# Performance work log

Hardware: AMD Instinct MI355X
Metric: run time of the kernel (lower is better)

## Reference

```python
import jax, jax.numpy as jnp
import numpy as np

TEMPERATURE = 8.0  # init_kwargs temperature
NEG_INF = -1e16


def setup_inputs() -> dict:
    key = jax.random.key(0)
    ks = jax.random.split(key, 8)
    B, S, D = 4, 1024, 64
    q = jax.random.normal(ks[0], (B, S, D), dtype=jnp.float32)
    k = jax.random.normal(ks[1], (B, S, D), dtype=jnp.float32)
    v = jax.random.normal(ks[2], (B, S, D), dtype=jnp.float32)
    # MLP params (Linear(2D,50) -> ReLU -> Linear(50,25) -> ReLU -> Linear(25,1))
    W1 = jax.random.normal(ks[3], (2 * D, 50), dtype=jnp.float32) * (1.0 / np.sqrt(2 * D))
    b1 = jnp.zeros((50,), dtype=jnp.float32)
    W2 = jax.random.normal(ks[4], (50, 25), dtype=jnp.float32) * (1.0 / np.sqrt(50))
    b2 = jnp.zeros((25,), dtype=jnp.float32)
    W3 = jax.random.normal(ks[5], (25, 1), dtype=jnp.float32) * (1.0 / np.sqrt(25))
    b3 = jnp.zeros((1,), dtype=jnp.float32)
    # causal mask: True where attention is disallowed (j > i)
    mask = jnp.triu(jnp.ones((S, S), dtype=bool), k=1)
    mask = jnp.broadcast_to(mask, (B, S, S))
    return {"q": q, "k": k, "v": v, "W1": W1, "b1": b1, "W2": W2,
            "b2": b2, "W3": W3, "b3": b3, "mask": mask}


def reference(q, k, v, W1, b1, W2, b2, W3, b3, mask):
    D = q.shape[-1]
    # cat([q_i, k_j]) @ W1 == q_i @ W1[:D] + k_j @ W1[D:]; avoids the
    # explicit [B,S,S,2D] concat the torch code materializes.
    Wq, Wk = W1[:D], W1[D:]
    hq = jnp.einsum('bsd,df->bsf', q, Wq)           # [B,S,50]
    hk = jnp.einsum('btd,df->btf', k, Wk)           # [B,S,50]
    h1 = jax.nn.relu(hq[:, :, None, :] + hk[:, None, :, :] + b1)  # [B,S,S,50]
    h2 = jax.nn.relu(jnp.einsum('bstf,fg->bstg', h1, W2) + b2)    # [B,S,S,25]
    scores = (jnp.einsum('bstg,go->bsto', h2, W3) + b3)[..., 0]    # [B,S,S]
    scores = scores / TEMPERATURE
    scores = jnp.where(mask, NEG_INF, scores)
    attn = jax.nn.softmax(scores, axis=2)           # softmax over key dim
    out = jnp.einsum('bst,btd->bsd', attn, v)       # [B,S,D]
    return (out, attn)
```

## Files before the change

kernel.cpp:

```cpp
#include <hip/hip_runtime.h>
#include <hip/hip_fp16.h>
#include <math.h>

#define BB 4
#define SQL 1024
#define DD 64
#define NFP 64
#define TEMP_INV 0.125f

typedef __attribute__((ext_vector_type(8))) _Float16 f16x8;
typedef __attribute__((ext_vector_type(4))) float f32x4;

__global__ __launch_bounds__(256) void proj_kernel(
    const float* __restrict__ q, const float* __restrict__ k,
    const float* __restrict__ W1, const float* __restrict__ b1,
    _Float16* __restrict__ hq, _Float16* __restrict__ hk)
{
  const int lane = threadIdx.x & 63;
  const int wave = threadIdx.x >> 6;
  const int unit = blockIdx.x * 4 + wave;
  const int isK  = unit >> 12;
  const int row  = unit & 4095;
  __shared__ float r[4][DD];
  const float* src = isK ? k : q;
  r[wave][lane] = src[row * DD + lane];
  __syncthreads();
  float acc = 0.f;
  if (lane < 50) {
    acc = isK ? 0.f : b1[lane];
    const float* w = W1 + isK * DD * 50 + lane;
#pragma unroll
    for (int d = 0; d < DD; ++d) acc = fmaf(r[wave][d], w[d * 50], acc);
  }
  _Float16* dst = isK ? hk : hq;
  dst[row * NFP + lane] = (_Float16)acc;
}

__global__ __launch_bounds__(512, 4) void attn_kernel(
    const _Float16* __restrict__ hq, const _Float16* __restrict__ hk,
    const float* __restrict__ v,
    const float* __restrict__ W2, const float* __restrict__ b2,
    const float* __restrict__ W3, const float* __restrict__ b3,
    float* __restrict__ out, float* __restrict__ attn)
{
  const int bid  = blockIdx.x;
  const int b    = blockIdx.y;
  const int tid  = threadIdx.x;
  const int lane = tid & 63;
  const int wave = tid >> 6;
  const int lo   = lane & 15;
  const int grp  = lane >> 4;

  __shared__ float sc[8][SQL];
  __shared__ _Float16 shq[8][NFP];

  const int sA = 4 * bid;
  const int sB = 1020 - 4 * bid;

  if (tid < 64) {
    int r = tid >> 3, c8 = (tid & 7) * 8;
    int s = (r < 4) ? (sA + r) : (sB + r - 4);
    *(float4*)(&shq[r][c8]) =
        *(const float4*)(hq + ((size_t)(b * SQL + s)) * NFP + c8);
  }

  f16x8 w2f[2][2];
#pragma unroll
  for (int gt = 0; gt < 2; ++gt) {
    int g = lo + 16 * gt;
#pragma unroll
    for (int c = 0; c < 2; ++c) {
      f16x8 fr;
#pragma unroll
      for (int j = 0; j < 8; ++j) {
        int f = c * 32 + grp * 8 + j;
        float val = (f < 50 && g < 25) ? W2[f * 25 + g] : 0.f;
        fr[j] = (_Float16)val;
      }
      w2f[gt][c] = fr;
    }
  }
  float w3a[4], w3b[4], b2a[4], b2b[4];
#pragma unroll
  for (int rr = 0; rr < 4; ++rr) {
    int g0 = grp * 4 + rr;
    int g1 = 16 + grp * 4 + rr;
    w3a[rr] = W3[g0];
    b2a[rr] = b2[g0];
    w3b[rr] = (g1 < 25) ? W3[g1] : 0.f;
    b2b[rr] = (g1 < 25) ? b2[g1] : 0.f;
  }
  const float b3v = b3[0];

  __syncthreads();

  const int smax = sB + 3;
  const int ntiles = (smax >> 5) + 1;
  const _Float16* hkb = hk + (size_t)b * SQL * NFP;

  for (int tt = wave; tt < ntiles; tt += 8) {
    const int tbase = tt << 5;
    f16x8 hkv[2][2];
#pragma unroll
    for (int th = 0; th < 2; ++th) {
      const _Float16* p = hkb + (size_t)(tbase + th * 16 + lo) * NFP + grp * 8;
#pragma unroll
      for (int c = 0; c < 2; ++c)
        hkv[th][c] = *(const f16x8*)(p + c * 32);
    }
#pragma unroll 1
    for (int r = 0; r < 8; ++r) {
      const int s = (r < 4) ? (sA + r) : (sB + r - 4);
      if (s < tbase) continue;
      f16x8 hqv[2];
#pragma unroll
      for (int c = 0; c < 2; ++c)
        hqv[c] = *(const f16x8*)(&shq[r][c * 32 + grp * 8]);
      f32x4 acc[2][2] = {{{0.f,0.f,0.f,0.f},{0.f,0.f,0.f,0.f}},
                         {{0.f,0.f,0.f,0.f},{0.f,0.f,0.f,0.f}}};
#pragma unroll
      for (int th = 0; th < 2; ++th) {
#pragma unroll
        for (int c = 0; c < 2; ++c) {
          f16x8 h = hqv[c] + hkv[th][c];
          f16x8 bfrag = __builtin_elementwise_max(h, (f16x8)0);
          acc[th][0] = __builtin_amdgcn_mfma_f32_16x16x32_f16(w2f[0][c], bfrag, acc[th][0], 0, 0, 0);
          acc[th][1] = __builtin_amdgcn_mfma_f32_16x16x32_f16(w2f[1][c], bfrag, acc[th][1], 0, 0, 0);
        }
      }
#pragma unroll
      for (int th = 0; th < 2; ++th) {
        float part = 0.f;
#pragma unroll
        for (int rr = 0; rr < 4; ++rr) {
          part += fmaxf(acc[th][0][rr] + b2a[rr], 0.f) * w3a[rr];
          part += fmaxf(acc[th][1][rr] + b2b[rr], 0.f) * w3b[rr];
        }
        part += __shfl_xor(part, 16);
        part += __shfl_xor(part, 32);
        float score = (part + b3v) * TEMP_INV;
        if (lane < 16) sc[r][tbase + th * 16 + lane] = score;
      }
    }
  }

  __syncthreads();

  {
    const int r = wave;
    const int s = (r < 4) ? (sA + r) : (sB + r - 4);
    float vv[16];
#pragma unroll
    for (int c = 0; c < 16; ++c) {
      int t = c * 64 + lane;
      vv[c] = (t <= s) ? sc[r][t] : -INFINITY;
    }
    float m = vv[0];
#pragma unroll
    for (int c = 1; c < 16; ++c) m = fmaxf(m, vv[c]);
#pragma unroll
    for (int off = 32; off; off >>= 1) m = fmaxf(m, __shfl_xor(m, off));
    float sum = 0.f;
#pragma unroll
    for (int c = 0; c < 16; ++c) {
      float e = (c * 64 + lane <= s) ? __expf(vv[c] - m) : 0.f;
      vv[c] = e;
      sum += e;
    }
#pragma unroll
    for (int off = 32; off; off >>= 1) sum += __shfl_xor(sum, off);
    const float inv = 1.f / sum;
    float* arow = attn + ((size_t)(b * SQL + s)) * SQL;
#pragma unroll
    for (int c = 0; c < 16; ++c) {
      float a = vv[c] * inv;
      arow[c * 64 + lane] = a;
      sc[r][c * 64 + lane] = a;
    }
    const float* vb = v + (size_t)(b * SQL) * DD + lane;
    float a0 = 0.f, a1 = 0.f, a2 = 0.f, a3 = 0.f;
    int t = 0;
    for (; t + 3 <= s; t += 4) {
      a0 = fmaf(sc[r][t],     vb[(size_t)(t)     * DD], a0);
      a1 = fmaf(sc[r][t + 1], vb[(size_t)(t + 1) * DD], a1);
      a2 = fmaf(sc[r][t + 2], vb[(size_t)(t + 2) * DD], a2);
      a3 = fmaf(sc[r][t + 3], vb[(size_t)(t + 3) * DD], a3);
    }
    for (; t <= s; ++t) a0 = fmaf(sc[r][t], vb[(size_t)t * DD], a0);
    out[((size_t)(b * SQL + s)) * DD + lane] = (a0 + a1) + (a2 + a3);
  }
}

extern "C" void kernel_launch(void* const* d_in, const int* in_sizes, int n_in,
                              void* d_out, int out_size, void* d_ws, size_t ws_size,
                              hipStream_t stream) {
  const float* q  = (const float*)d_in[0];
  const float* k  = (const float*)d_in[1];
  const float* v  = (const float*)d_in[2];
  const float* W1 = (const float*)d_in[3];
  const float* b1 = (const float*)d_in[4];
  const float* W2 = (const float*)d_in[5];
  const float* b2 = (const float*)d_in[6];
  const float* W3 = (const float*)d_in[7];
  const float* b3 = (const float*)d_in[8];

  float* out  = (float*)d_out;
  float* attn = out + BB * SQL * DD;

  _Float16* hq = (_Float16*)d_ws;
  _Float16* hk = hq + BB * SQL * NFP;

  proj_kernel<<<dim3(2048), 256, 0, stream>>>(q, k, W1, b1, hq, hk);
  attn_kernel<<<dim3(128, BB), 512, 0, stream>>>(hq, hk, v, W2, b2, W3, b3, out, attn);
}
```

Measured before the change: 177.0 us.

## Split attention into score and softmax-PV kernels with global score buffer

The fused attention kernel becomes two kernels. The score kernel spreads the key tiles of each block over twice as many blocks and handles the low and high query rows of a pair together, so each loaded hk tile is reused. It writes scores to a global workspace buffer. A new per-row kernel then does softmax and the PV product with 256 threads, splitting the key range across waves. This removes the serial single-wave softmax/PV tail and the large shared score array, but adds a 16 MB round trip to global memory and one more launch.

Measured after the change: 155.9 us. 1.14x faster.

```diff
diff --git a/kernel.cpp b/kernel.cpp
--- a/kernel.cpp
+++ b/kernel.cpp
@@ -25,33 +25,35 @@
   const float* src = isK ? k : q;
   r[wave][lane] = src[row * DD + lane];
   __syncthreads();
-  float acc = 0.f;
+  float acc0 = 0.f, acc1 = 0.f;
   if (lane < 50) {
-    acc = isK ? 0.f : b1[lane];
+    acc0 = isK ? 0.f : b1[lane];
     const float* w = W1 + isK * DD * 50 + lane;
 #pragma unroll
-    for (int d = 0; d < DD; ++d) acc = fmaf(r[wave][d], w[d * 50], acc);
+    for (int d = 0; d < DD; d += 2) {
+      acc0 = fmaf(r[wave][d],     w[d * 50],       acc0);
+      acc1 = fmaf(r[wave][d + 1], w[(d + 1) * 50], acc1);
+    }
   }
   _Float16* dst = isK ? hk : hq;
-  dst[row * NFP + lane] = (_Float16)acc;
-}
-
-__global__ __launch_bounds__(512, 4) void attn_kernel(
+  dst[row * NFP + lane] = (_Float16)(acc0 + acc1);
+}
+
+__global__ __launch_bounds__(512, 4) void score_kernel(
     const _Float16* __restrict__ hq, const _Float16* __restrict__ hk,
-    const float* __restrict__ v,
     const float* __restrict__ W2, const float* __restrict__ b2,
     const float* __restrict__ W3, const float* __restrict__ b3,
-    float* __restrict__ out, float* __restrict__ attn)
+    float* __restrict__ sc_g)
 {
   const int bid  = blockIdx.x;
-  const int b    = blockIdx.y;
+  const int half = blockIdx.y;
+  const int b    = blockIdx.z;
   const int tid  = threadIdx.x;
   const int lane = tid & 63;
   const int wave = tid >> 6;
   const int lo   = lane & 15;
   const int grp  = lane >> 4;
 
-  __shared__ float sc[8][SQL];
   __shared__ _Float16 shq[8][NFP];
 
   const int sA = 4 * bid;
@@ -94,11 +96,10 @@
 
   __syncthreads();
 
-  const int smax = sB + 3;
-  const int ntiles = (smax >> 5) + 1;
+  const int ntiles = ((sB + 3) >> 5) + 1;
   const _Float16* hkb = hk + (size_t)b * SQL * NFP;
 
-  for (int tt = wave; tt < ntiles; tt += 8) {
+  for (int tt = wave + (half << 3); tt < ntiles; tt += 16) {
     const int tbase = tt << 5;
     f16x8 hkv[2][2];
 #pragma unroll
@@ -109,86 +110,145 @@
         hkv[th][c] = *(const f16x8*)(p + c * 32);
     }
 #pragma unroll 1
-    for (int r = 0; r < 8; ++r) {
-      const int s = (r < 4) ? (sA + r) : (sB + r - 4);
-      if (s < tbase) continue;
-      f16x8 hqv[2];
+    for (int pr = 0; pr < 4; ++pr) {
+      const int s_h = sB + pr;
+      if (s_h < tbase) continue;
+      const int s_l = sA + pr;
+      const bool has_l = (s_l >= tbase);
+
+      f16x8 hqh[2], hql[2];
 #pragma unroll
       for (int c = 0; c < 2; ++c)
-        hqv[c] = *(const f16x8*)(&shq[r][c * 32 + grp * 8]);
-      f32x4 acc[2][2] = {{{0.f,0.f,0.f,0.f},{0.f,0.f,0.f,0.f}},
-                         {{0.f,0.f,0.f,0.f},{0.f,0.f,0.f,0.f}}};
+        hqh[c] = *(const f16x8*)(&shq[pr + 4][c * 32 + grp * 8]);
+      if (has_l) {
+#pragma unroll
+        for (int c = 0; c < 2; ++c)
+          hql[c] = *(const f16x8*)(&shq[pr][c * 32 + grp * 8]);
+      }
+
+      f32x4 acch[2][2] = {{{0.f,0.f,0.f,0.f},{0.f,0.f,0.f,0.f}},
+                          {{0.f,0.f,0.f,0.f},{0.f,0.f,0.f,0.f}}};
+      f32x4 accl[2][2] = {{{0.f,0.f,0.f,0.f},{0.f,0.f,0.f,0.f}},
+                          {{0.f,0.f,0.f,0.f},{0.f,0.f,0.f,0.f}}};
 #pragma unroll
       for (int th = 0; th < 2; ++th) {
 #pragma unroll
         for (int c = 0; c < 2; ++c) {
-          f16x8 h = hqv[c] + hkv[th][c];
-          f16x8 bfrag = __builtin_elementwise_max(h, (f16x8)0);
-          acc[th][0] = __builtin_amdgcn_mfma_f32_16x16x32_f16(w2f[0][c], bfrag, acc[th][0], 0, 0, 0);
-          acc[th][1] = __builtin_amdgcn_mfma_f32_16x16x32_f16(w2f[1][c], bfrag, acc[th][1], 0, 0, 0);
+          f16x8 bh = __builtin_elementwise_max(hqh[c] + hkv[th][c], (f16x8)0);
+          acch[th][0] = __builtin_amdgcn_mfma_f32_16x16x32_f16(w2f[0][c], bh, acch[th][0], 0, 0, 0);
+          acch[th][1] = __builtin_amdgcn_mfma_f32_16x16x32_f16(w2f[1][c], bh, acch[th][1], 0, 0, 0);
+          if (has_l) {
+            f16x8 bl = __builtin_elementwise_max(hql[c] + hkv[th][c], (f16x8)0);
+            accl[th][0] = __builtin_amdgcn_mfma_f32_16x16x32_f16(w2f[0][c], bl, accl[th][0], 0, 0, 0);
+            accl[th][1] = __builtin_amdgcn_mfma_f32_16x16x32_f16(w2f[1][c], bl, accl[th][1], 0, 0, 0);
+          }
         }
       }
+      float sh[2], sl[2];
 #pragma unroll
       for (int th = 0; th < 2; ++th) {
         float part = 0.f;
 #pragma unroll
         for (int rr = 0; rr < 4; ++rr) {
-          part += fmaxf(acc[th][0][rr] + b2a[rr], 0.f) * w3a[rr];
-          part += fmaxf(acc[th][1][rr] + b2b[rr], 0.f) * w3b[rr];
+          part += fmaxf(acch[th][0][rr] + b2a[rr], 0.f) * w3a[rr];
+          part += fmaxf(acch[th][1][rr] + b2b[rr], 0.f) * w3b[rr];
         }
         part += __shfl_xor(part, 16);
         part += __shfl_xor(part, 32);
-        float score = (part + b3v) * TEMP_INV;
-        if (lane < 16) sc[r][tbase + th * 16 + lane] = score;
-      }
-    }
-  }
-
-  __syncthreads();
-
-  {
-    const int r = wave;
-    const int s = (r < 4) ? (sA + r) : (sB + r - 4);
-    float vv[16];
-#pragma unroll
-    for (int c = 0; c < 16; ++c) {
-      int t = c * 64 + lane;
-      vv[c] = (t <= s) ? sc[r][t] : -INFINITY;
-    }
-    float m = vv[0];
-#pragma unroll
-    for (int c = 1; c < 16; ++c) m = fmaxf(m, vv[c]);
-#pragma unroll
-    for (int off = 32; off; off >>= 1) m = fmaxf(m, __shfl_xor(m, off));
-    float sum = 0.f;
-#pragma unroll
-    for (int c = 0; c < 16; ++c) {
-      float e = (c * 64 + lane <= s) ? __expf(vv[c] - m) : 0.f;
-      vv[c] = e;
-      sum += e;
-    }
-#pragma unroll
-    for (int off = 32; off; off >>= 1) sum += __shfl_xor(sum, off);
-    const float inv = 1.f / sum;
-    float* arow = attn + ((size_t)(b * SQL + s)) * SQL;
-#pragma unroll
-    for (int c = 0; c < 16; ++c) {
-      float a = vv[c] * inv;
-      arow[c * 64 + lane] = a;
-      sc[r][c * 64 + lane] = a;
-    }
-    const float* vb = v + (size_t)(b * SQL) * DD + lane;
-    float a0 = 0.f, a1 = 0.f, a2 = 0.f, a3 = 0.f;
-    int t = 0;
-    for (; t + 3 <= s; t += 4) {
-      a0 = fmaf(sc[r][t],     vb[(size_t)(t)     * DD], a0);
-      a1 = fmaf(sc[r][t + 1], vb[(size_t)(t + 1) * DD], a1);
-      a2 = fmaf(sc[r][t + 2], vb[(size_t)(t + 2) * DD], a2);
-      a3 = fmaf(sc[r][t + 3], vb[(size_t)(t + 3) * DD], a3);
-    }
-    for (; t <= s; ++t) a0 = fmaf(sc[r][t], vb[(size_t)t * DD], a0);
-    out[((size_t)(b * SQL + s)) * DD + lane] = (a0 + a1) + (a2 + a3);
-  }
+        sh[th] = (part + b3v) * TEMP_INV;
+      }
+      if (lane < 32)
+        sc_g[((size_t)(b * SQL + s_h) << 10) + tbase + lane] = (lane & 16) ? sh[1] : sh[0];
+      if (has_l) {
+#pragma unroll
+        for (int th = 0; th < 2; ++th) {
+          float part = 0.f;
+#pragma unroll
+          for (int rr = 0; rr < 4; ++rr) {
+            part += fmaxf(accl[th][0][rr] + b2a[rr], 0.f) * w3a[rr];
+            part += fmaxf(accl[th][1][rr] + b2b[rr], 0.f) * w3b[rr];
+          }
+          part += __shfl_xor(part, 16);
+          part += __shfl_xor(part, 32);
+          sl[th] = (part + b3v) * TEMP_INV;
+        }
+        if (lane < 32)
+          sc_g[((size_t)(b * SQL + s_l) << 10) + tbase + lane] = (lane & 16) ? sl[1] : sl[0];
+      }
+    }
+  }
+}
+
+__global__ __launch_bounds__(256) void smpv_kernel(
+    const float* __restrict__ sc_g, const float* __restrict__ v,
+    float* __restrict__ out, float* __restrict__ attn)
+{
+  const int s    = blockIdx.x;
+  const int b    = blockIdx.y;
+  const int tid  = threadIdx.x;
+  const int lane = tid & 63;
+  const int wave = tid >> 6;
+
+  __shared__ float sp[SQL];
+  __shared__ float red[2][4];
+  __shared__ float outred[4][DD];
+
+  const float* srow = sc_g + ((size_t)(b * SQL + s) << 10);
+
+  float vv[4];
+  float m = -INFINITY;
+#pragma unroll
+  for (int c = 0; c < 4; ++c) {
+    int t = tid + c * 256;
+    vv[c] = (t <= s) ? srow[t] : -INFINITY;
+    m = fmaxf(m, vv[c]);
+  }
+#pragma unroll
+  for (int off = 32; off; off >>= 1) m = fmaxf(m, __shfl_xor(m, off));
+  if (lane == 0) red[0][wave] = m;
+  __syncthreads();
+  m = fmaxf(fmaxf(red[0][0], red[0][1]), fmaxf(red[0][2], red[0][3]));
+
+  float sum = 0.f;
+#pragma unroll
+  for (int c = 0; c < 4; ++c) {
+    float e = (tid + c * 256 <= s) ? __expf(vv[c] - m) : 0.f;
+    vv[c] = e;
+    sum += e;
+  }
+#pragma unroll
+  for (int off = 32; off; off >>= 1) sum += __shfl_xor(sum, off);
+  if (lane == 0) red[1][wave] = sum;
+  __syncthreads();
+  sum = red[1][0] + red[1][1] + red[1][2] + red[1][3];
+  const float inv = 1.f / sum;
+
+  float* arow = attn + ((size_t)(b * SQL + s)) * SQL;
+#pragma unroll
+  for (int c = 0; c < 4; ++c) {
+    float a = vv[c] * inv;
+    arow[tid + c * 256] = a;
+    sp[tid + c * 256] = a;
+  }
+  __syncthreads();
+
+  const int cs = ((((s + 1) + 3) >> 2) + 3) & ~3;
+  const int t0 = wave * cs;
+  const int te = min((wave + 1) * cs, SQL);
+  const float* vb = v + (size_t)(b * SQL) * DD + lane;
+  float a0 = 0.f, a1 = 0.f, a2 = 0.f, a3 = 0.f;
+  for (int t = t0; t < te; t += 4) {
+    float4 av = *(const float4*)(&sp[t]);
+    a0 = fmaf(av.x, vb[(size_t)(t)     * DD], a0);
+    a1 = fmaf(av.y, vb[(size_t)(t + 1) * DD], a1);
+    a2 = fmaf(av.z, vb[(size_t)(t + 2) * DD], a2);
+    a3 = fmaf(av.w, vb[(size_t)(t + 3) * DD], a3);
+  }
+  outred[wave][lane] = (a0 + a1) + (a2 + a3);
+  __syncthreads();
+  if (tid < DD)
+    out[((size_t)(b * SQL + s)) * DD + tid] =
+        outred[0][tid] + outred[1][tid] + outred[2][tid] + outred[3][tid];
 }
 
 extern "C" void kernel_launch(void* const* d_in, const int* in_sizes, int n_in,
@@ -207,9 +267,11 @@
   float* out  = (float*)d_out;
   float* attn = out + BB * SQL * DD;
 
-  _Float16* hq = (_Float16*)d_ws;
+  float* sc_g = (float*)d_ws;
+  _Float16* hq = (_Float16*)(sc_g + (size_t)BB * SQL * SQL);
   _Float16* hk = hq + BB * SQL * NFP;
 
   proj_kernel<<<dim3(2048), 256, 0, stream>>>(q, k, W1, b1, hq, hk);
-  attn_kernel<<<dim3(128, BB), 512, 0, stream>>>(hq, hk, v, W2, b2, W3, b3, out, attn);
-}
+  score_kernel<<<dim3(128, 2, BB), 512, 0, stream>>>(hq, hk, W2, b2, W3, b3, sc_g);
+  smpv_kernel<<<dim3(SQL, BB), 256, 0, stream>>>(sc_g, v, out, attn);
+}
```
